# Kernel tuning notes

Measured on AMD Instinct MI355X. Metric: run time of the kernel, lower is better.

Reference implementation:

```python
import jax, jax.numpy as jnp
import numpy as np


def setup_inputs() -> dict:
    key = jax.random.key(0)
    B, A, C, H, W = 16, 3, 80, 76, 76
    output = jax.random.normal(key, (B, (C + 5) * A, H, W), dtype=jnp.float32)
    # anchors are divided by stride in the module's __init__ (stride=8)
    anchors = jnp.array([[10.0, 13.0], [16.0, 30.0], [33.0, 23.0]], dtype=jnp.float32) / 8.0
    return {"output": output, "anchors": anchors}


def reference(output, anchors):
    # Dense YOLO grid decode (get_region_boxes without the data-dependent
    # threshold extraction, which just filters these values on CPU).
    B, c, H, W = output.shape
    A = anchors.shape[0]
    C = c // A - 5
    out = output.reshape(B, A, C + 5, H, W)  # anchor-major channel groups
    anchors = jax.lax.stop_gradient(anchors)  # matches Aw.detach()/Ah.detach()

    gx = jnp.arange(W, dtype=output.dtype)            # [W], broadcast over H
    gy = jnp.arange(H, dtype=output.dtype)[:, None]   # [H,1]
    aw = anchors[:, 0][None, :, None, None]           # [1,A,1,1]
    ah = anchors[:, 1][None, :, None, None]

    xs = (jax.nn.sigmoid(out[:, :, 0]) + gx) / W      # [B,A,H,W] normalized cx
    ys = (jax.nn.sigmoid(out[:, :, 1]) + gy) / H
    ws = (jnp.exp(out[:, :, 2]) * aw) / W
    hs = (jnp.exp(out[:, :, 3]) * ah) / H
    conf = jax.nn.sigmoid(out[:, :, 4])

    cls_logits = out[:, :, 5:]                        # [B,A,C,H,W]
    cls_conf = jax.lax.stop_gradient(jax.nn.softmax(cls_logits, axis=2))  # .detach()
    cls_prob = jnp.max(cls_conf, axis=2)              # [B,A,H,W]
    cls_id = jax.lax.stop_gradient(
        jnp.argmax(cls_conf, axis=2).astype(output.dtype))

    # [B,A,H,W,7]: cx, cy, w, h, box_conf, cls_prob, cls_id (as float)
    boxes = jnp.stack([xs, ys, ws, hs, conf, cls_prob, cls_id], axis=-1)
    return boxes
```

## Files before the change

### kernel.cpp

```cpp
#include <hip/hip_runtime.h>


#define B_  16
#define A_  3
#define C_  80
#define H_  76
#define W_  76
#define PLANE (H_ * W_)
#define CPW  20

__device__ __forceinline__ float fast_exp(float x) {
    return __builtin_amdgcn_exp2f(x * 1.44269504088896340736f);
}

__device__ __forceinline__ float fast_rcp(float x) {
    return __builtin_amdgcn_rcpf(x);
}

__device__ __forceinline__ float sigmoidf(float x) {
    return fast_rcp(1.0f + fast_exp(-x));
}

__global__ __launch_bounds__(256) void yolo_kernel(const float* __restrict__ in,
                                                   const float* __restrict__ anchors,
                                                   float* __restrict__ out) {
    const int tid  = threadIdx.x;
    const int lane = tid & 63;
    const int wid  = tid >> 6;
    const int a = blockIdx.y;
    const int b = blockIdx.z;
    const int pos_base = blockIdx.x * 64;
    const int pos  = pos_base + lane;
    const int posc = (pos < PLANE) ? pos : (PLANE - 1);

    const float* base = in + (size_t)((b * A_ + a) * (C_ + 5)) * PLANE + posc;

    const float* cb = base + (size_t)(5 + wid * CPW) * PLANE;
    float l[CPW];
    #pragma unroll
    for (int j = 0; j < CPW; ++j) l[j] = cb[(size_t)j * PLANE];

    float t0 = 0.f, t1 = 0.f, t2 = 0.f, t3 = 0.f, t4 = 0.f;
    if (wid == 0) {
        t0 = base[0 * PLANE];
        t1 = base[1 * PLANE];
        t2 = base[2 * PLANE];
        t3 = base[3 * PLANE];
        t4 = base[4 * PLANE];
    }

    float m = l[0];
    int   id = 0;
    #pragma unroll
    for (int j = 1; j < CPW; ++j) {
        if (l[j] > m) { m = l[j]; id = j; }
    }
    float s = 0.0f;
    #pragma unroll
    for (int j = 0; j < CPW; ++j) s += fast_exp(l[j] - m);

    __shared__ float sm[4][64];
    __shared__ float ss[4][64];
    __shared__ int   sid[4][64];
    __shared__ float res[64 * 7];

    sm[wid][lane]  = m;
    ss[wid][lane]  = s;
    sid[wid][lane] = id + wid * CPW;
    __syncthreads();

    if (wid == 0) {
        float M  = sm[0][lane];
        int   ID = sid[0][lane];
        #pragma unroll
        for (int w = 1; w < 4; ++w) {
            const float mw = sm[w][lane];
            if (mw > M) { M = mw; ID = sid[w][lane]; }
        }
        float S = 0.0f;
        #pragma unroll
        for (int w = 0; w < 4; ++w) S += ss[w][lane] * fast_exp(sm[w][lane] - M);

        const int x = posc % W_;
        const int y = posc / W_;
        const float aw = anchors[2 * a + 0];
        const float ah = anchors[2 * a + 1];

        res[lane * 7 + 0] = (sigmoidf(t0) + (float)x) * (1.0f / (float)W_);
        res[lane * 7 + 1] = (sigmoidf(t1) + (float)y) * (1.0f / (float)H_);
        res[lane * 7 + 2] = fast_exp(t2) * aw * (1.0f / (float)W_);
        res[lane * 7 + 3] = fast_exp(t3) * ah * (1.0f / (float)H_);
        res[lane * 7 + 4] = sigmoidf(t4);
        res[lane * 7 + 5] = fast_rcp(S);
        res[lane * 7 + 6] = (float)ID;
    }
    __syncthreads();

    const size_t obase = (size_t)((b * A_ + a) * PLANE + pos_base) * 7;
    #pragma unroll
    for (int k = 0; k < 2; ++k) {
        const int f = tid + k * 256;
        if (f < 64 * 7 && (pos_base + f / 7) < PLANE) {
            out[obase + f] = res[f];
        }
    }
}

extern "C" void kernel_launch(void* const* d_in, const int* in_sizes, int n_in,
                              void* d_out, int out_size, void* d_ws, size_t ws_size,
                              hipStream_t stream) {
    const float* in      = (const float*)d_in[0];
    const float* anchors = (const float*)d_in[1];
    float* out           = (float*)d_out;

    dim3 grid((PLANE + 63) / 64, A_, B_);
    dim3 block(256, 1, 1);
    yolo_kernel<<<grid, block, 0, stream>>>(in, anchors, out);
}
```

Before: 138.0 us.

## Process four positions per thread with float4 loads and online softmax

```diff
diff --git a/kernel.cpp b/kernel.cpp
--- a/kernel.cpp
+++ b/kernel.cpp
@@ -8,6 +8,8 @@
 #define W_  76
 #define PLANE (H_ * W_)
 #define CPW  20
+#define PPL  4
+#define PPB  256
 
 __device__ __forceinline__ float fast_exp(float x) {
     return __builtin_amdgcn_exp2f(x * 1.44269504088896340736f);
@@ -21,88 +23,102 @@
     return fast_rcp(1.0f + fast_exp(-x));
 }
 
-__global__ __launch_bounds__(256) void yolo_kernel(const float* __restrict__ in,
-                                                   const float* __restrict__ anchors,
-                                                   float* __restrict__ out) {
+__global__ __launch_bounds__(256, 4) void yolo_kernel(const float* __restrict__ in,
+                                                      const float* __restrict__ anchors,
+                                                      float* __restrict__ out) {
     const int tid  = threadIdx.x;
     const int lane = tid & 63;
     const int wid  = tid >> 6;
     const int a = blockIdx.y;
     const int b = blockIdx.z;
-    const int pos_base = blockIdx.x * 64;
-    const int pos  = pos_base + lane;
-    const int posc = (pos < PLANE) ? pos : (PLANE - 1);
+    const int pos_base = blockIdx.x * PPB;
+    const int p0  = pos_base + lane * PPL;
+    const int p0c = (p0 <= PLANE - PPL) ? p0 : (PLANE - PPL);
 
-    const float* base = in + (size_t)((b * A_ + a) * (C_ + 5)) * PLANE + posc;
+    const float* base = in + (size_t)((b * A_ + a) * (C_ + 5)) * PLANE + p0c;
+    const float* cb   = base + (size_t)(5 + wid * CPW) * PLANE;
 
-    const float* cb = base + (size_t)(5 + wid * CPW) * PLANE;
-    float l[CPW];
+    float m[PPL], s[PPL];
+    int   id[PPL];
+    {
+        const float4 v0 = *(const float4*)cb;
+        m[0] = v0.x; m[1] = v0.y; m[2] = v0.z; m[3] = v0.w;
+        #pragma unroll
+        for (int k = 0; k < PPL; ++k) { s[k] = 1.0f; id[k] = 0; }
+    }
     #pragma unroll
-    for (int j = 0; j < CPW; ++j) l[j] = cb[(size_t)j * PLANE];
-
-    float t0 = 0.f, t1 = 0.f, t2 = 0.f, t3 = 0.f, t4 = 0.f;
-    if (wid == 0) {
-        t0 = base[0 * PLANE];
-        t1 = base[1 * PLANE];
-        t2 = base[2 * PLANE];
-        t3 = base[3 * PLANE];
-        t4 = base[4 * PLANE];
+    for (int j = 1; j < CPW; ++j) {
+        const float4 vj = *(const float4*)(cb + (size_t)j * PLANE);
+        const float lv[PPL] = {vj.x, vj.y, vj.z, vj.w};
+        #pragma unroll
+        for (int k = 0; k < PPL; ++k) {
+            const float mn = fmaxf(m[k], lv[k]);
+            s[k] = s[k] * fast_exp(m[k] - mn) + fast_exp(lv[k] - mn);
+            if (lv[k] > m[k]) id[k] = j;
+            m[k] = mn;
+        }
     }
 
-    float m = l[0];
-    int   id = 0;
-    #pragma unroll
-    for (int j = 1; j < CPW; ++j) {
-        if (l[j] > m) { m = l[j]; id = j; }
+    float tb[5][PPL];
+    if (wid == 0) {
+        #pragma unroll
+        for (int c = 0; c < 5; ++c) {
+            const float4 v = *(const float4*)(base + (size_t)c * PLANE);
+            tb[c][0] = v.x; tb[c][1] = v.y; tb[c][2] = v.z; tb[c][3] = v.w;
+        }
     }
-    float s = 0.0f;
-    #pragma unroll
-    for (int j = 0; j < CPW; ++j) s += fast_exp(l[j] - m);
 
-    __shared__ float sm[4][64];
-    __shared__ float ss[4][64];
-    __shared__ int   sid[4][64];
-    __shared__ float res[64 * 7];
+    __shared__ __align__(16) float sm[4][64][PPL];
+    __shared__ __align__(16) float ss[4][64][PPL];
+    __shared__ __align__(16) int   sd[4][64][PPL];
+    __shared__ __align__(16) float res[PPB * 7];
 
-    sm[wid][lane]  = m;
-    ss[wid][lane]  = s;
-    sid[wid][lane] = id + wid * CPW;
+    *(float4*)sm[wid][lane] = make_float4(m[0], m[1], m[2], m[3]);
+    *(float4*)ss[wid][lane] = make_float4(s[0], s[1], s[2], s[3]);
+    *(int4*)  sd[wid][lane] = make_int4(id[0] + wid * CPW, id[1] + wid * CPW,
+                                        id[2] + wid * CPW, id[3] + wid * CPW);
     __syncthreads();
 
     if (wid == 0) {
-        float M  = sm[0][lane];
-        int   ID = sid[0][lane];
+        const float aw = anchors[2 * a + 0] * (1.0f / (float)W_);
+        const float ah = anchors[2 * a + 1] * (1.0f / (float)H_);
         #pragma unroll
-        for (int w = 1; w < 4; ++w) {
-            const float mw = sm[w][lane];
-            if (mw > M) { M = mw; ID = sid[w][lane]; }
+        for (int k = 0; k < PPL; ++k) {
+            float M  = sm[0][lane][k];
+            int   ID = sd[0][lane][k];
+            #pragma unroll
+            for (int w = 1; w < 4; ++w) {
+                const float mw = sm[w][lane][k];
+                if (mw > M) { M = mw; ID = sd[w][lane][k]; }
+            }
+            float S = 0.0f;
+            #pragma unroll
+            for (int w = 0; w < 4; ++w) S += ss[w][lane][k] * fast_exp(sm[w][lane][k] - M);
+
+            const int p = p0c + k;
+            const int x = p % W_;
+            const int y = p / W_;
+            float* r = &res[(lane * PPL + k) * 7];
+            r[0] = (sigmoidf(tb[0][k]) + (float)x) * (1.0f / (float)W_);
+            r[1] = (sigmoidf(tb[1][k]) + (float)y) * (1.0f / (float)H_);
+            r[2] = fast_exp(tb[2][k]) * aw;
+            r[3] = fast_exp(tb[3][k]) * ah;
+            r[4] = sigmoidf(tb[4][k]);
+            r[5] = fast_rcp(S);
+            r[6] = (float)ID;
         }
-        float S = 0.0f;
-        #pragma unroll
-        for (int w = 0; w < 4; ++w) S += ss[w][lane] * fast_exp(sm[w][lane] - M);
-
-        const int x = posc % W_;
-        const int y = posc / W_;
-        const float aw = anchors[2 * a + 0];
-        const float ah = anchors[2 * a + 1];
-
-        res[lane * 7 + 0] = (sigmoidf(t0) + (float)x) * (1.0f / (float)W_);
-        res[lane * 7 + 1] = (sigmoidf(t1) + (float)y) * (1.0f / (float)H_);
-        res[lane * 7 + 2] = fast_exp(t2) * aw * (1.0f / (float)W_);
-        res[lane * 7 + 3] = fast_exp(t3) * ah * (1.0f / (float)H_);
-        res[lane * 7 + 4] = sigmoidf(t4);
-        res[lane * 7 + 5] = fast_rcp(S);
-        res[lane * 7 + 6] = (float)ID;
     }
     __syncthreads();
 
+    const int nvalid = (PLANE - pos_base < PPB) ? (PLANE - pos_base) : PPB;
+    const int n4 = nvalid * 7 / 4;
     const size_t obase = (size_t)((b * A_ + a) * PLANE + pos_base) * 7;
+    float4* out4 = (float4*)(out + obase);
+    const float4* res4 = (const float4*)res;
     #pragma unroll
-    for (int k = 0; k < 2; ++k) {
-        const int f = tid + k * 256;
-        if (f < 64 * 7 && (pos_base + f / 7) < PLANE) {
-            out[obase + f] = res[f];
-        }
+    for (int t = 0; t < 2; ++t) {
+        const int idx = tid + t * 256;
+        if (idx < n4) out4[idx] = res4[idx];
     }
 }
 
@@ -113,7 +129,7 @@
     const float* anchors = (const float*)d_in[1];
     float* out           = (float*)d_out;
 
-    dim3 grid((PLANE + 63) / 64, A_, B_);
+    dim3 grid((PLANE + PPB - 1) / PPB, A_, B_);
     dim3 block(256, 1, 1);
     yolo_kernel<<<grid, block, 0, stream>>>(in, anchors, out);
 }
```

Result: slower. 141.0 us (+2.2%).
